# Kernel tuning notes

Measured on AMD Instinct MI355X. Metric: run time of the kernel, lower is better.

## Reference

```python
import jax, jax.numpy as jnp
import numpy as np

B, I, O, NB, H = 32768, 256, 256, 256, 16  # batch, input_dim, output_dim, num_basis, hidden

def setup_inputs() -> dict:
    key = jax.random.key(0)
    ks = jax.random.split(key, 6)
    x = jax.random.normal(ks[0], (B, I), dtype=jnp.float32)
    weights = jax.random.normal(ks[1], (O, I, NB), dtype=jnp.float32)
    # Stacked per-input-dim basis MLPs: Linear(1,16) -> SiLU -> Linear(16,1)
    # Kaiming-uniform-ish init scale; exact init irrelevant for correctness baseline
    w1 = jax.random.normal(ks[2], (I, H), dtype=jnp.float32)          # Linear(1,16).weight squeezed
    b1 = jax.random.normal(ks[3], (I, H), dtype=jnp.float32) * 0.1
    w2 = jax.random.normal(ks[4], (I, H), dtype=jnp.float32) / np.sqrt(H)  # Linear(16,1).weight squeezed
    b2 = jax.random.normal(ks[5], (I,), dtype=jnp.float32) * 0.1
    return {"x": x, "weights": weights, "w1": w1, "b1": b1, "w2": w2, "b2": b2}

def reference(x, weights, w1, b1, w2, b2):
    # phi_i(x[:, i]) for all i at once. hidden: [B, I, H]
    hidden = jax.nn.silu(x[:, :, None] * w1[None, :, :] + b1[None, :, :])
    phi = jnp.einsum('bih,ih->bi', hidden, w2) + b2[None, :]  # [B, I]
    # weight * basis_output summed over last dim == sum_k weights[o,i,k] * phi
    wsum = jnp.sum(weights, axis=-1)  # [O, I]
    return jnp.einsum('bi,oi->bo', phi, wsum)  # [B, O]
```

## Files before the change

### kernel.cpp

```cpp
#include <hip/hip_runtime.h>


#define B_DIM 32768
#define I_DIM 256
#define O_DIM 256
#define NB_DIM 256

typedef __bf16 bf16x8 __attribute__((ext_vector_type(8)));
typedef float f32x4 __attribute__((ext_vector_type(4)));

__global__ __launch_bounds__(256) void k_prep(
    const float* __restrict__ wt,
    const float* __restrict__ x,
    const float* __restrict__ w1,
    const float* __restrict__ b1,
    const float* __restrict__ w2,
    const float* __restrict__ b2,
    __bf16* __restrict__ wpack,
    __bf16* __restrict__ phi)
{
    const unsigned b = blockIdx.x;
    if (b % 5u == 0u) {
        const int i = (int)threadIdx.x;
        float w1r[16], b1r[16], w2r[16];
        #pragma unroll
        for (int q = 0; q < 4; ++q) {
            const float4 a = ((const float4*)(w1 + i * 16))[q];
            const float4 c = ((const float4*)(b1 + i * 16))[q];
            const float4 d = ((const float4*)(w2 + i * 16))[q];
            w1r[q*4+0] = a.x; w1r[q*4+1] = a.y; w1r[q*4+2] = a.z; w1r[q*4+3] = a.w;
            b1r[q*4+0] = c.x; b1r[q*4+1] = c.y; b1r[q*4+2] = c.z; b1r[q*4+3] = c.w;
            w2r[q*4+0] = d.x; w2r[q*4+1] = d.y; w2r[q*4+2] = d.z; w2r[q*4+3] = d.w;
        }
        const float b2r = b2[i];
        const int r0 = (int)(b / 5u) * 32;
        float xv = x[(size_t)r0 * I_DIM + i];
        for (int rr = 0; rr < 32; ++rr) {
            const int r = r0 + rr;
            const float xn = (rr < 31) ? x[(size_t)(r + 1) * I_DIM + i] : 0.0f;
            float acc = b2r;
            #pragma unroll
            for (int h = 0; h < 16; ++h) {
                const float z = fmaf(xv, w1r[h], b1r[h]);
                const float sg = __builtin_amdgcn_rcpf(
                    1.0f + __builtin_amdgcn_exp2f(z * -1.44269504f));
                acc = fmaf(z * sg, w2r[h], acc);
            }
            phi[(size_t)r * I_DIM + i] = (__bf16)acc;
            xv = xn;
        }
    } else {
        const unsigned wb = b - b / 5u - 1u;
        const int wave = (int)(threadIdx.x >> 6);
        const int lane = (int)(threadIdx.x & 63u);
        const int pbase = ((int)wb * 4 + wave) * 4;
        #pragma unroll
        for (int j = 0; j < 4; ++j) {
            const int p = pbase + j;
            const float4 v = ((const float4*)(wt + (size_t)p * NB_DIM))[lane];
            float s = (v.x + v.y) + (v.z + v.w);
            #pragma unroll
            for (int off = 32; off; off >>= 1) s += __shfl_down(s, off, 64);
            if (lane == 0) {
                const int o = p >> 8, ii = p & 255;
                const int l = (o & 15) + (((ii >> 3) & 3) << 4);
                wpack[(size_t)((((o >> 4) * 8 + (ii >> 5)) * 64) + l) * 8 + (ii & 7)] =
                    (__bf16)s;
            }
        }
    }
}

__global__ __launch_bounds__(512) void k_gemm(
    const __bf16* __restrict__ phi,
    const __bf16* __restrict__ wpack,
    float* __restrict__ out)
{
    __shared__ uint4 atile4[2048];
    char* atile = (char*)atile4;
    const int tid = (int)threadIdx.x;
    const int lane = tid & 63, wave = tid >> 6;
    const int wm = wave >> 2, wn = wave & 3;

    const char* src = (const char*)phi + (size_t)blockIdx.x * 32768;
    #pragma unroll
    for (int it = 0; it < 4; ++it) {
        const int off = it * 8192 + tid * 16;
        const uint4 v = *(const uint4*)(src + off);
        const int swz = off ^ (((off >> 9) & 7) << 4);
        *(uint4*)(atile + swz) = v;
    }
    __syncthreads();

    const int rowsel = lane & 15;
    const int kgrp = lane >> 4;
    f32x4 acc[2][4] = {};
    #pragma unroll
    for (int kx = 0; kx < 8; ++kx) {
        bf16x8 a[2], bb[4];
        #pragma unroll
        for (int t = 0; t < 2; ++t) {
            const int r = wm * 32 + t * 16 + rowsel;
            const int i0 = kx * 32 + kgrp * 8;
            const int boff = (r << 9) + (((i0 << 1)) ^ ((r & 7) << 4));
            a[t] = *(const bf16x8*)(atile + boff);
        }
        #pragma unroll
        for (int t = 0; t < 4; ++t) {
            const int nf = wn * 4 + t;
            bb[t] = *(const bf16x8*)(wpack + (size_t)(((nf * 8 + kx) * 64) + lane) * 8);
        }
        #pragma unroll
        for (int mi = 0; mi < 2; ++mi)
            #pragma unroll
            for (int ni = 0; ni < 4; ++ni)
                acc[mi][ni] = __builtin_amdgcn_mfma_f32_16x16x32_bf16(
                    a[mi], bb[ni], acc[mi][ni], 0, 0, 0);
    }

    const int m_base = (int)blockIdx.x * 64 + wm * 32;
    const int n_base = wn * 64;
    const int r0 = (lane >> 4) * 4, c = lane & 15;
    #pragma unroll
    for (int mi = 0; mi < 2; ++mi)
        #pragma unroll
        for (int ni = 0; ni < 4; ++ni)
            #pragma unroll
            for (int rr = 0; rr < 4; ++rr)
                out[(size_t)(m_base + mi * 16 + r0 + rr) * O_DIM + n_base + ni * 16 + c] =
                    acc[mi][ni][rr];
}

extern "C" void kernel_launch(void* const* d_in, const int* in_sizes, int n_in,
                              void* d_out, int out_size, void* d_ws, size_t ws_size,
                              hipStream_t stream) {
    const float* x  = (const float*)d_in[0];
    const float* wt = (const float*)d_in[1];
    const float* w1 = (const float*)d_in[2];
    const float* b1 = (const float*)d_in[3];
    const float* w2 = (const float*)d_in[4];
    const float* b2 = (const float*)d_in[5];
    float* out = (float*)d_out;

    __bf16* wpack = (__bf16*)d_ws;
    __bf16* phi   = (__bf16*)((char*)d_ws + 256 * 1024);

    hipLaunchKernelGGL(k_prep, dim3(5120), dim3(256), 0, stream,
                       wt, x, w1, b1, w2, b2, wpack, phi);
    hipLaunchKernelGGL(k_gemm, dim3(512), dim3(512), 0, stream,
                       phi, wpack, out);
}
```

Before: 189.2 us.

## Fuse basis MLP computation into GEMM kernel, split weight-sum into separate kernel

The phi computation (the per-input SiLU MLP) now runs inside the GEMM kernel and writes bf16 results straight into the swizzled LDS A-tile, so the phi intermediate no longer round-trips through global memory. The weight-sum reduction becomes its own kernel, launched before the fused kernel. This removes the 16 MB phi write and read, but puts the transcendental-heavy MLP on the GEMM's critical path with only 512 blocks of parallelism. It also adds a second dependent launch and loses the overlap the interleaved prep kernel had.

```diff
diff --git a/kernel.cpp b/kernel.cpp
--- a/kernel.cpp
+++ b/kernel.cpp
@@ -9,91 +9,91 @@
 typedef __bf16 bf16x8 __attribute__((ext_vector_type(8)));
 typedef float f32x4 __attribute__((ext_vector_type(4)));
 
-__global__ __launch_bounds__(256) void k_prep(
+__device__ __forceinline__ size_t wpack_idx(int o, int ii) {
+    const int l = (o & 15) | (((ii >> 3) & 3) << 4);
+    return (size_t)((((o >> 4) * 8 + (ii >> 5)) * 64) + l) * 8 + (ii & 7);
+}
+
+__global__ __launch_bounds__(256) void k_wsum(
     const float* __restrict__ wt,
+    __bf16* __restrict__ wpack)
+{
+    const int wave = (int)(threadIdx.x >> 6);
+    const int lane = (int)(threadIdx.x & 63u);
+    const int pbase = ((int)blockIdx.x * 4 + wave) * 4;
+    #pragma unroll
+    for (int j = 0; j < 4; ++j) {
+        const int p = pbase + j;
+        const float4 v = ((const float4*)(wt + (size_t)p * NB_DIM))[lane];
+        float s = (v.x + v.y) + (v.z + v.w);
+        #pragma unroll
+        for (int off = 32; off; off >>= 1) s += __shfl_down(s, off, 64);
+        if (lane == 0) wpack[wpack_idx(p >> 8, p & 255)] = (__bf16)s;
+    }
+}
+
+__global__ __launch_bounds__(512, 4) void k_fused(
     const float* __restrict__ x,
     const float* __restrict__ w1,
     const float* __restrict__ b1,
     const float* __restrict__ w2,
     const float* __restrict__ b2,
-    __bf16* __restrict__ wpack,
-    __bf16* __restrict__ phi)
-{
-    const unsigned b = blockIdx.x;
-    if (b % 5u == 0u) {
-        const int i = (int)threadIdx.x;
-        float w1r[16], b1r[16], w2r[16];
-        #pragma unroll
-        for (int q = 0; q < 4; ++q) {
-            const float4 a = ((const float4*)(w1 + i * 16))[q];
-            const float4 c = ((const float4*)(b1 + i * 16))[q];
-            const float4 d = ((const float4*)(w2 + i * 16))[q];
-            w1r[q*4+0] = a.x; w1r[q*4+1] = a.y; w1r[q*4+2] = a.z; w1r[q*4+3] = a.w;
-            b1r[q*4+0] = c.x; b1r[q*4+1] = c.y; b1r[q*4+2] = c.z; b1r[q*4+3] = c.w;
-            w2r[q*4+0] = d.x; w2r[q*4+1] = d.y; w2r[q*4+2] = d.z; w2r[q*4+3] = d.w;
-        }
-        const float b2r = b2[i];
-        const int r0 = (int)(b / 5u) * 32;
-        float xv = x[(size_t)r0 * I_DIM + i];
-        for (int rr = 0; rr < 32; ++rr) {
-            const int r = r0 + rr;
-            const float xn = (rr < 31) ? x[(size_t)(r + 1) * I_DIM + i] : 0.0f;
-            float acc = b2r;
-            #pragma unroll
-            for (int h = 0; h < 16; ++h) {
-                const float z = fmaf(xv, w1r[h], b1r[h]);
-                const float sg = __builtin_amdgcn_rcpf(
-                    1.0f + __builtin_amdgcn_exp2f(z * -1.44269504f));
-                acc = fmaf(z * sg, w2r[h], acc);
-            }
-            phi[(size_t)r * I_DIM + i] = (__bf16)acc;
-            xv = xn;
-        }
-    } else {
-        const unsigned wb = b - b / 5u - 1u;
-        const int wave = (int)(threadIdx.x >> 6);
-        const int lane = (int)(threadIdx.x & 63u);
-        const int pbase = ((int)wb * 4 + wave) * 4;
-        #pragma unroll
-        for (int j = 0; j < 4; ++j) {
-            const int p = pbase + j;
-            const float4 v = ((const float4*)(wt + (size_t)p * NB_DIM))[lane];
-            float s = (v.x + v.y) + (v.z + v.w);
-            #pragma unroll
-            for (int off = 32; off; off >>= 1) s += __shfl_down(s, off, 64);
-            if (lane == 0) {
-                const int o = p >> 8, ii = p & 255;
-                const int l = (o & 15) + (((ii >> 3) & 3) << 4);
-                wpack[(size_t)((((o >> 4) * 8 + (ii >> 5)) * 64) + l) * 8 + (ii & 7)] =
-                    (__bf16)s;
-            }
-        }
-    }
-}
-
-__global__ __launch_bounds__(512) void k_gemm(
-    const __bf16* __restrict__ phi,
     const __bf16* __restrict__ wpack,
     float* __restrict__ out)
 {
     __shared__ uint4 atile4[2048];
     char* atile = (char*)atile4;
     const int tid = (int)threadIdx.x;
-    const int lane = tid & 63, wave = tid >> 6;
-    const int wm = wave >> 2, wn = wave & 3;
 
-    const char* src = (const char*)phi + (size_t)blockIdx.x * 32768;
-    #pragma unroll
-    for (int it = 0; it < 4; ++it) {
-        const int off = it * 8192 + tid * 16;
-        const uint4 v = *(const uint4*)(src + off);
-        const int swz = off ^ (((off >> 9) & 7) << 4);
-        *(uint4*)(atile + swz) = v;
+    {
+        const int i = tid & 255;
+        const int half = tid >> 8;
+        const float4* w1v = (const float4*)(w1 + i * 16);
+        const float4* b1v = (const float4*)(b1 + i * 16);
+        const float4* w2v = (const float4*)(w2 + i * 16);
+        const float4 w1a = w1v[0], w1b = w1v[1], w1c = w1v[2], w1d = w1v[3];
+        const float4 b1a = b1v[0], b1b = b1v[1], b1c = b1v[2], b1d = b1v[3];
+        const float4 w2a = w2v[0], w2b = w2v[1], w2c = w2v[2], w2d = w2v[3];
+        const float b2r = b2[i];
+        const size_t xbase = (size_t)((int)blockIdx.x * 64 + half * 32) * I_DIM + i;
+
+        for (int rr = 0; rr < 32; rr += 2) {
+            const float xv0 = x[xbase + (size_t)rr * I_DIM];
+            const float xv1 = x[xbase + (size_t)(rr + 1) * I_DIM];
+            float acc0 = b2r, acc1 = b2r;
+#define KAN_STEP(WV, BV, DV)                                                   \
+            {                                                                  \
+                float z0 = fmaf(xv0, WV, BV), z1 = fmaf(xv1, WV, BV);          \
+                float s0 = __builtin_amdgcn_rcpf(                              \
+                    1.0f + __builtin_amdgcn_exp2f(z0 * -1.44269504f));         \
+                float s1 = __builtin_amdgcn_rcpf(                              \
+                    1.0f + __builtin_amdgcn_exp2f(z1 * -1.44269504f));         \
+                acc0 = fmaf(z0 * s0, DV, acc0);                                \
+                acc1 = fmaf(z1 * s1, DV, acc1);                                \
+            }
+            KAN_STEP(w1a.x, b1a.x, w2a.x) KAN_STEP(w1a.y, b1a.y, w2a.y)
+            KAN_STEP(w1a.z, b1a.z, w2a.z) KAN_STEP(w1a.w, b1a.w, w2a.w)
+            KAN_STEP(w1b.x, b1b.x, w2b.x) KAN_STEP(w1b.y, b1b.y, w2b.y)
+            KAN_STEP(w1b.z, b1b.z, w2b.z) KAN_STEP(w1b.w, b1b.w, w2b.w)
+            KAN_STEP(w1c.x, b1c.x, w2c.x) KAN_STEP(w1c.y, b1c.y, w2c.y)
+            KAN_STEP(w1c.z, b1c.z, w2c.z) KAN_STEP(w1c.w, b1c.w, w2c.w)
+            KAN_STEP(w1d.x, b1d.x, w2d.x) KAN_STEP(w1d.y, b1d.y, w2d.y)
+            KAN_STEP(w1d.z, b1d.z, w2d.z) KAN_STEP(w1d.w, b1d.w, w2d.w)
+#undef KAN_STEP
+            const int rl0 = half * 32 + rr, rl1 = rl0 + 1;
+            const int a0 = (rl0 * 512 + i * 2) ^ ((rl0 & 7) << 4);
+            const int a1 = (rl1 * 512 + i * 2) ^ ((rl1 & 7) << 4);
+            *(__bf16*)(atile + a0) = (__bf16)acc0;
+            *(__bf16*)(atile + a1) = (__bf16)acc1;
+        }
     }
     __syncthreads();
 
+    const int lane = tid & 63, wave = tid >> 6;
+    const int wm = wave >> 2, wn = wave & 3;
     const int rowsel = lane & 15;
     const int kgrp = lane >> 4;
+
     f32x4 acc[2][4] = {};
     #pragma unroll
     for (int kx = 0; kx < 8; ++kx) {
@@ -101,8 +101,7 @@
         #pragma unroll
         for (int t = 0; t < 2; ++t) {
             const int r = wm * 32 + t * 16 + rowsel;
-            const int i0 = kx * 32 + kgrp * 8;
-            const int boff = (r << 9) + (((i0 << 1)) ^ ((r & 7) << 4));
+            const int boff = (r << 9) + ((kx * 64 + kgrp * 16) ^ ((r & 7) << 4));
             a[t] = *(const bf16x8*)(atile + boff);
         }
         #pragma unroll
@@ -143,10 +142,8 @@
     float* out = (float*)d_out;
 
     __bf16* wpack = (__bf16*)d_ws;
-    __bf16* phi   = (__bf16*)((char*)d_ws + 256 * 1024);
 
-    hipLaunchKernelGGL(k_prep, dim3(5120), dim3(256), 0, stream,
-                       wt, x, w1, b1, w2, b2, wpack, phi);
-    hipLaunchKernelGGL(k_gemm, dim3(512), dim3(512), 0, stream,
-                       phi, wpack, out);
+    hipLaunchKernelGGL(k_wsum, dim3(4096), dim3(256), 0, stream, wt, wpack);
+    hipLaunchKernelGGL(k_fused, dim3(512), dim3(512), 0, stream,
+                       x, w1, b1, w2, b2, wpack, out);
 }
```

Measured after the change: 170.9 us. 1.11x faster.
